# Performance work log

Measured on AMD Instinct MI355X. Metric: run time of the kernel, lower is better.

Reference implementation:

```python
import jax, jax.numpy as jnp
import numpy as np
from jax import lax

IMG_SIZE = 1024
NUM_CLASSES = 80
TOP_K = 300          # self.top_k
CLS_THRES = 0.05     # self.cls_thres
IOU_THR = 0.5        # nms overlap
BBOX_STD = jnp.array([0.1, 0.1, 0.2, 0.2], dtype=jnp.float32)


def make_anchors(img_size=IMG_SIZE):
    """Standard RetinaNet anchors: P3-P7, 3 ratios x 3 scales per cell."""
    strides = [8, 16, 32, 64, 128]
    ratios = np.array([0.5, 1.0, 2.0])
    scales = 2.0 ** (np.arange(3) / 3.0)
    out = []
    for s in strides:
        base = 4.0 * s
        ws, hs = [], []
        for r in ratios:
            for sc in scales:
                ws.append(base * sc / np.sqrt(r))
                hs.append(base * sc * np.sqrt(r))
        ws = np.array(ws); hs = np.array(hs)  # [9]
        fs = img_size // s
        shift = (np.arange(fs) + 0.5) * s
        cy, cx = np.meshgrid(shift, shift, indexing='ij')
        cx = cx.ravel()[:, None]; cy = cy.ravel()[:, None]
        a = np.stack([cx - ws / 2, cy - hs / 2, cx + ws / 2, cy + hs / 2], axis=-1)
        out.append(a.reshape(-1, 4))
    return np.concatenate(out, axis=0).astype(np.float32)  # [A,4]


def setup_inputs() -> dict:
    key = jax.random.key(0)
    k1, k2 = jax.random.split(key)
    anchors = jnp.asarray(make_anchors())[None]          # [1,A,4]
    A = anchors.shape[1]
    classifications = jax.random.uniform(k1, (1, A, NUM_CLASSES), dtype=jnp.float32)
    regressions = jax.random.normal(k2, (1, A, 4), dtype=jnp.float32)
    return {"classifications": classifications, "regressions": regressions,
            "anchors": anchors, "img_h": IMG_SIZE, "img_w": IMG_SIZE}


def decode_boxes(anchors, regressions):
    # BBoxTransform: mean=0, std=[.1,.1,.2,.2]
    w = anchors[..., 2] - anchors[..., 0]
    h = anchors[..., 3] - anchors[..., 1]
    cx = anchors[..., 0] + 0.5 * w
    cy = anchors[..., 1] + 0.5 * h
    d = regressions * BBOX_STD
    pcx = cx + d[..., 0] * w
    pcy = cy + d[..., 1] * h
    pw = jnp.exp(d[..., 2]) * w
    ph = jnp.exp(d[..., 3]) * h
    return jnp.stack([pcx - 0.5 * pw, pcy - 0.5 * ph,
                      pcx + 0.5 * pw, pcy + 0.5 * ph], axis=-1)


def pairwise_iou(b):  # b: [K,4]
    x1, y1, x2, y2 = b[:, 0], b[:, 1], b[:, 2], b[:, 3]
    area = jnp.clip(x2 - x1, 0) * jnp.clip(y2 - y1, 0)
    iw = jnp.clip(jnp.minimum(x2[:, None], x2[None]) - jnp.maximum(x1[:, None], x1[None]), 0)
    ih = jnp.clip(jnp.minimum(y2[:, None], y2[None]) - jnp.maximum(y1[:, None], y1[None]), 0)
    inter = iw * ih
    return inter / (area[:, None] + area[None] - inter + 1e-8)


def nms_one_class(boxes, scores_c):
    """Greedy NMS over top-K candidates above threshold for one class."""
    s = jnp.where(scores_c > CLS_THRES, scores_c, -jnp.inf)
    top_scores, top_idx = lax.top_k(s, TOP_K)        # sorted descending
    cand_valid = top_scores > CLS_THRES
    iou = pairwise_iou(boxes[top_idx])               # [K,K]
    idxs = jnp.arange(TOP_K)

    def body(suppressed, i):
        sup_i = suppressed[i] | (~cand_valid[i])
        new_sup = suppressed | ((~sup_i) & (iou[i] > IOU_THR) & (idxs > i))
        return new_sup, ~sup_i

    _, keep = lax.scan(body, jnp.zeros(TOP_K, bool), idxs)
    return top_idx, top_scores, keep


def reference(classifications, regressions, anchors, img_h, img_w):
    boxes = decode_boxes(anchors, regressions)       # [1,A,4]
    boxes = jnp.stack([jnp.maximum(boxes[..., 0], 0.0),
                       jnp.maximum(boxes[..., 1], 0.0),
                       jnp.minimum(boxes[..., 2], float(img_w)),
                       jnp.minimum(boxes[..., 3], float(img_h))], axis=-1)
    boxes0 = boxes[0]                                # [A,4]  (batch item 0, as original)
    cls0 = classifications[0]                        # [A,C]
    A, C = cls0.shape

    # per-class NMS, vmapped over the class axis
    top_idx, top_scores, keep = jax.vmap(nms_one_class, in_axes=(None, 1))(boxes0, cls0)
    # scatter kept scores back into dense [A,C] matrix (original 'scores' tensor)
    scores_mat = jnp.zeros((A, C), cls0.dtype).at[top_idx, jnp.arange(C)[:, None]].set(
        jnp.where(keep, top_scores, 0.0))

    scores_max = scores_mat.max(axis=1)
    labels = scores_mat.argmax(axis=1)
    valid = scores_max > 0
    # fixed-shape (jit-friendly) equivalent of the original's boolean filtering:
    final_scores = jnp.where(valid, scores_max, 0.0)
    final_labels = jnp.where(valid, labels, -1)
    final_boxes = jnp.where(valid[:, None], boxes0, 0.0)
    return final_scores, final_labels, final_boxes
```

## Files before the change

kernel.cpp:

```cpp
#include <hip/hip_runtime.h>
#include <cstdint>

typedef unsigned long long u64;
typedef unsigned int u32;

#define CLS_T    0.05f
#define T1G      0.9965f
#define TOPK     300
#define NWORDS   5
#define HBINS    2560
#define KEY_BASE 0x3D000000u
#define CCAP     1024
#define NBLK     2048
#define SCAP     16
#define OVBIT    0x80000000u

__device__ inline u32 bin_of_bits(u32 bits) {
    u32 b = (bits - KEY_BASE) >> 14;
    if (b > (HBINS - 1)) b = HBINS - 1;
    return b;
}

__device__ inline void cex(u64& v, u64 p, bool lo, bool up) {
    u64 mx = v > p ? v : p;
    u64 mn = v > p ? p : v;
    v = (lo == up) ? mx : mn;
}
__device__ inline void sstep(u64& a0, u64& a1, u32 tid, u32 kk, u32 j) {
    u64 p0 = __shfl_xor((unsigned long long)a0, (int)j, 64);
    u64 p1 = __shfl_xor((unsigned long long)a1, (int)j, 64);
    bool lo = ((tid & j) == 0);
    cex(a0, p0, lo, ((tid & kk) == 0));
    cex(a1, p1, lo, (((tid + 512u) & kk) == 0));
}
__device__ inline void lstep640(u64* cand, u64& a0, u64& a1, u32 tid, u32 kk, u32 j) {
    __syncthreads();
    if (tid < 512) { cand[tid] = a0; cand[tid + 512] = a1; }
    __syncthreads();
    if (tid < 512) {
        u64 p0 = cand[tid ^ j], p1 = cand[(tid ^ j) + 512];
        bool lo = ((tid & j) == 0);
        cex(a0, p0, lo, ((tid & kk) == 0));
        cex(a1, p1, lo, (((tid + 512u) & kk) == 0));
    }
}

__global__ void decode_kernel(const float* __restrict__ anc,
                              const float* __restrict__ reg,
                              const int* __restrict__ ph,
                              const int* __restrict__ pw,
                              float* __restrict__ boxes,
                              u64* __restrict__ akey, int A)
{
    int a = blockIdx.x * blockDim.x + threadIdx.x;
    if (a >= A) return;
    akey[a] = 0;
    float x1 = anc[a*4+0], y1 = anc[a*4+1], x2 = anc[a*4+2], y2 = anc[a*4+3];
    float w = x2 - x1, h = y2 - y1;
    float cx = x1 + 0.5f*w, cy = y1 + 0.5f*h;
    float r0 = reg[a*4+0]*0.1f, r1 = reg[a*4+1]*0.1f;
    float r2 = reg[a*4+2]*0.2f, r3 = reg[a*4+3]*0.2f;
    float pcx = cx + r0*w, pcy = cy + r1*h;
    float pw_ = expf(r2)*w, ph_ = expf(r3)*h;
    float W = (float)(*pw), H = (float)(*ph);
    boxes[a*4+0] = fmaxf(pcx - 0.5f*pw_, 0.0f);
    boxes[a*4+1] = fmaxf(pcy - 0.5f*ph_, 0.0f);
    boxes[a*4+2] = fminf(pcx + 0.5f*pw_, W);
    boxes[a*4+3] = fminf(pcy + 0.5f*ph_, H);
}

__global__ __launch_bounds__(256) void fused_scan_kernel(
    const float* __restrict__ anc, const float* __restrict__ reg,
    const int* __restrict__ ph, const int* __restrict__ pw,
    const float* __restrict__ cls,
    float* __restrict__ boxes, u64* __restrict__ akey,
    u64* __restrict__ gbuf, u32* __restrict__ segcnt, int A)
{
    const int tid = threadIdx.x;
    const int blk = blockIdx.x;

    float W = (float)(*pw), H = (float)(*ph);
    for (int a = blk * 256 + tid; a < A; a += NBLK * 256) {
        akey[a] = 0;
        float x1 = anc[a*4+0], y1 = anc[a*4+1], x2 = anc[a*4+2], y2 = anc[a*4+3];
        float w = x2 - x1, h = y2 - y1;
        float cx = x1 + 0.5f*w, cy = y1 + 0.5f*h;
        float r0 = reg[a*4+0]*0.1f, r1 = reg[a*4+1]*0.1f;
        float r2 = reg[a*4+2]*0.2f, r3 = reg[a*4+3]*0.2f;
        float pcx = cx + r0*w, pcy = cy + r1*h;
        float pw_ = expf(r2)*w, ph_ = expf(r3)*h;
        boxes[a*4+0] = fmaxf(pcx - 0.5f*pw_, 0.0f);
        boxes[a*4+1] = fmaxf(pcy - 0.5f*ph_, 0.0f);
        boxes[a*4+2] = fminf(pcx + 0.5f*pw_, W);
        boxes[a*4+3] = fminf(pcy + 0.5f*ph_, H);
    }

    __shared__ u32 cnt[80];
    __shared__ u64 buf[80][SCAP];
    __shared__ u32 s_over;
    for (int i = tid; i < 80; i += 256) cnt[i] = 0;
    if (tid == 0) s_over = 0;
    __syncthreads();

    size_t Nf4 = (size_t)A * 20;
    const float4* p4 = (const float4*)cls;
    for (size_t i = (size_t)blk * 256 + tid; i < Nf4; i += (size_t)NBLK * 256) {
        float4 v = p4[i];
        float ss[4] = {v.x, v.y, v.z, v.w};
        #pragma unroll
        for (int q = 0; q < 4; ++q) {
            if (ss[q] > T1G) {
                u32 flat = (u32)(i * 4 + q);
                u32 a = flat / 80u;
                u32 c = flat - a * 80u;
                u32 p = atomicAdd(&cnt[c], 1u);
                if (p < SCAP) buf[c][p] = ((u64)__float_as_uint(ss[q]) << 32) | (u32)(~a);
                else s_over = 1;
            }
        }
    }
    __syncthreads();

    const u32 ob = s_over ? OVBIT : 0u;
    for (int m = tid; m < 80 * SCAP; m += 256) {
        int c = m / SCAP, e = m - c * SCAP;
        u32 cc = cnt[c]; if (cc > SCAP) cc = SCAP;
        if ((u32)e < cc)
            gbuf[((size_t)c * NBLK + blk) * SCAP + e] = buf[c][e];
    }
    for (int c = tid; c < 80; c += 256) {
        u32 cc = cnt[c]; if (cc > SCAP) cc = SCAP;
        segcnt[(size_t)c * NBLK + blk] = cc | ob;
    }
}

__global__ __launch_bounds__(256) void prefix_kernel(
    const u32* __restrict__ segcnt, u32* __restrict__ pref,
    u32* __restrict__ totals)
{
    const int c = blockIdx.x;
    const int tid = threadIdx.x;
    __shared__ u32 part[256];
    __shared__ u32 s_ob;
    if (tid == 0) s_ob = 0;
    __syncthreads();

    const u32* row = segcnt + (size_t)c * NBLK;
    u32 v[8];
    u32 s = 0, ob = 0;
    #pragma unroll
    for (int q = 0; q < 8; ++q) {
        u32 r = row[tid * 8 + q];
        ob |= r & OVBIT;
        v[q] = r & ~OVBIT;
        s += v[q];
    }
    if (ob) atomicOr(&s_ob, 1u);
    part[tid] = s;
    __syncthreads();
    for (int d = 1; d < 256; d <<= 1) {
        u32 t = (tid >= d) ? part[tid - d] : 0;
        __syncthreads();
        part[tid] += t;
        __syncthreads();
    }
    u32 running = part[tid] - s;
    u32* prow = pref + (size_t)c * NBLK;
    #pragma unroll
    for (int q = 0; q < 8; ++q) { prow[tid * 8 + q] = running; running += v[q]; }
    if (tid == 255) totals[c] = part[255] | (s_ob ? OVBIT : 0u);
}

__global__ __launch_bounds__(640) void class_fused_kernel(
    const u32* __restrict__ totals, const u32* __restrict__ pref,
    const u64* __restrict__ gbuf,
    const float* __restrict__ cls,
    const float* __restrict__ boxes, u64* __restrict__ akey, int A, int C)
{
    const int c = blockIdx.x;
    const u32 tid = threadIdx.x;
    const int lane = tid & 63;

    __shared__ u32 sh[HBINS];
    __shared__ u32 sp[NBLK];
    __shared__ u64 cand[CCAP];
    __shared__ u32 s_sel, s_cnt, s_rem;
    __shared__ float4 sbox[TOPK];
    __shared__ float  sbar[TOPK];
    __shared__ u64 iomaskT[NWORDS][TOPK];
    __shared__ u64 s_keep[NWORDS];

    if (tid == 0) { s_sel = 0; s_cnt = 0; }
    __syncthreads();

    const u32 traw = totals[c];
    const bool over = (traw & OVBIT) != 0;
    const u32 n = traw & ~OVBIT;
    u32 cnt_f = 0;
    bool fast_ok = false;

    if (!over && n >= TOPK && n <= CCAP) {
        for (int i = tid; i < NBLK; i += 640) sp[i] = pref[(size_t)c * NBLK + i];
        __syncthreads();
        for (u32 i = tid; i < n; i += 640) {
            int lo = 0, hi = NBLK;
            while (hi - lo > 1) {
                int mid = (lo + hi) >> 1;
                if (sp[mid] <= i) lo = mid; else hi = mid;
            }
            u32 e = i - sp[lo];
            cand[i] = gbuf[((size_t)c * NBLK + lo) * SCAP + e];
        }
        __syncthreads();
        cnt_f = n;
        fast_ok = true;
    }

    if (!fast_ok) {
        __syncthreads();
        for (int i = tid; i < HBINS; i += 640) sh[i] = 0;
        if (tid == 0) s_cnt = 0;
        __syncthreads();
        for (int a = tid; a < A; a += 640) {
            float s = cls[(size_t)a * C + c];
            if (s > CLS_T) atomicAdd(&sh[bin_of_bits(__float_as_uint(s))], 1u);
        }
        __syncthreads();
        if (tid == 0) {
            u32 cum = 0; int sel = 0;
            for (int d = HBINS - 1; d >= 0; --d) {
                u32 nc = cum + sh[d];
                if (nc >= TOPK) { sel = d; break; }
                cum = nc;
            }
            s_sel = (u32)sel; s_rem = TOPK - cum;
        }
        __syncthreads();
        const u32 sel1 = s_sel;
        __syncthreads();
        for (int i = tid; i < 256; i += 640) sh[i] = 0;
        __syncthreads();
        for (int a = tid; a < A; a += 640) {
            float s = cls[(size_t)a * C + c];
            if (s > CLS_T) {
                u32 k = __float_as_uint(s) - KEY_BASE;
                u32 b = k >> 14; if (b >= HBINS) b = HBINS - 1;
                if (b == sel1) atomicAdd(&sh[(k >> 6) & 0xFF], 1u);
            }
        }
        __syncthreads();
        if (tid == 0) {
            u32 rem = s_rem, cum = 0; int sel = 0;
            for (int d = 255; d >= 0; --d) {
                u32 nc = cum + sh[d];
                if (nc >= rem) { sel = d; break; }
                cum = nc;
            }
            s_sel = (sel1 << 14) | ((u32)sel << 6);
            s_cnt = 0;
        }
        __syncthreads();
        const u32 thresh = s_sel;
        for (int a = tid; a < A; a += 640) {
            float s = cls[(size_t)a * C + c];
            if (s > CLS_T) {
                u32 bits = __float_as_uint(s);
                if (bits - KEY_BASE >= thresh) {
                    u32 p = atomicAdd(&s_cnt, 1u);
                    if (p < CCAP) cand[p] = ((u64)bits << 32) | (u32)(~(u32)a);
                }
            }
        }
        __syncthreads();
        cnt_f = s_cnt < CCAP ? s_cnt : CCAP;
    }

    for (u32 i = cnt_f + tid; i < CCAP; i += 640) cand[i] = 0;
    for (int m = tid; m < NWORDS * TOPK; m += 640) ((u64*)iomaskT)[m] = 0;
    __syncthreads();

    u64 a0 = 0, a1 = 0;
    if (tid < 512) { a0 = cand[tid]; a1 = cand[tid + 512]; }
    if (tid < 512)
        for (u32 kk = 2; kk <= 64; kk <<= 1)
            for (u32 j = kk >> 1; j >= 1; j >>= 1)
                sstep(a0, a1, tid, kk, j);
    lstep640(cand, a0, a1, tid, 128u, 64u);
    if (tid < 512) for (u32 j = 32; j >= 1; j >>= 1) sstep(a0, a1, tid, 128u, j);
    lstep640(cand, a0, a1, tid, 256u, 128u);
    lstep640(cand, a0, a1, tid, 256u, 64u);
    if (tid < 512) for (u32 j = 32; j >= 1; j >>= 1) sstep(a0, a1, tid, 256u, j);
    lstep640(cand, a0, a1, tid, 512u, 256u);
    lstep640(cand, a0, a1, tid, 512u, 128u);
    lstep640(cand, a0, a1, tid, 512u, 64u);
    if (tid < 512) for (u32 j = 32; j >= 1; j >>= 1) sstep(a0, a1, tid, 512u, j);
    if (tid < 512) {
        u64 mx = a0 > a1 ? a0 : a1, mn = a0 > a1 ? a1 : a0;
        a0 = mx; a1 = mn;
    }
    lstep640(cand, a0, a1, tid, 1024u, 256u);
    lstep640(cand, a0, a1, tid, 1024u, 128u);
    lstep640(cand, a0, a1, tid, 1024u, 64u);
    if (tid < 512) for (u32 j = 32; j >= 1; j >>= 1) sstep(a0, a1, tid, 1024u, j);

    const int T = (int)(cnt_f < TOPK ? cnt_f : TOPK);

    u64 key = a0; u32 aidx = 0;
    if ((int)tid < T) {
        aidx = ~(u32)(key & 0xFFFFFFFFull);
        float4 b4 = *(const float4*)(boxes + (size_t)aidx * 4);
        sbox[tid] = b4;
        sbar[tid] = fmaxf(b4.z - b4.x, 0.0f) * fmaxf(b4.w - b4.y, 0.0f);
    }
    __syncthreads();

    {
        const int jj = (int)(tid < 320 ? tid : tid - 320);
        const int p  = (int)(tid < 320 ? 0 : 1);
        if (jj < T) {
            float4 b = sbox[jj];
            float ar = sbar[jj];
            u64 cm[NWORDS] = {0,0,0,0,0};
            for (int i = p; i < jj; i += 2) {
                float4 bi = sbox[i];
                float iw = fmaxf(fminf(b.z, bi.z) - fmaxf(b.x, bi.x), 0.0f);
                float ih = fmaxf(fminf(b.w, bi.w) - fmaxf(b.y, bi.y), 0.0f);
                float inter = iw * ih;
                float uni = ((ar + sbar[i]) - inter) + 1e-8f;
                if (inter / uni > 0.5f) cm[i >> 6] |= 1ull << (i & 63);
            }
            #pragma unroll
            for (int w = 0; w < NWORDS; ++w)
                if (cm[w]) atomicOr(&iomaskT[w][jj], cm[w]);
        }
    }
    __syncthreads();

    if (tid < 64) {
        u64 K[NWORDS];
        #pragma unroll
        for (int w = 0; w < NWORDS; ++w) {
            int b = w * 64 + lane;
            bool valid = (b < T);
            u64 cmw = 0, se = 0;
            if (valid) {
                #pragma unroll
                for (int w2 = 0; w2 < NWORDS; ++w2)
                    if (w2 < w) se |= K[w2] & iomaskT[w2][b];
                cmw = iomaskT[w][b];
            }
            u64 U = __ballot(valid && se == 0);
            u64 Kw = 0;
            int guard = 0;
            while (U && guard++ < 64) {
                u64 newk = __ballot(((U >> lane) & 1ull) && ((cmw & U) == 0));
                Kw |= newk; U &= ~newk;
                u64 supp = __ballot((cmw & Kw) != 0);
                U &= ~supp;
            }
            K[w] = Kw;
        }
        if (lane == 0) {
            #pragma unroll
            for (int w = 0; w < NWORDS; ++w) s_keep[w] = K[w];
        }
    }
    __syncthreads();

    if ((int)tid < T) {
        if ((s_keep[tid >> 6] >> (tid & 63)) & 1ull) {
            u32 sbits = (u32)(key >> 32);
            u64 outk = ((u64)sbits << 32) | (u32)(255 - c);
            atomicMax(&akey[aidx], outk);
        }
    }
}

__global__ void finalize_kernel(const u64* __restrict__ akey,
                                float* __restrict__ out, int A)
{
    int a = blockIdx.x * blockDim.x + threadIdx.x;
    if (a >= A) return;
    float* scores = out;
    float* labels = out + A;
    float* boxes  = out + (size_t)2 * A;
    u64 k = akey[a];
    if (k) {
        scores[a] = __uint_as_float((u32)(k >> 32));
        labels[a] = (float)(int)(255u - (u32)(k & 0xFFFFFFFFull));
    } else {
        scores[a] = 0.0f;
        labels[a] = -1.0f;
        boxes[(size_t)a*4+0] = 0.0f;
        boxes[(size_t)a*4+1] = 0.0f;
        boxes[(size_t)a*4+2] = 0.0f;
        boxes[(size_t)a*4+3] = 0.0f;
    }
}

#define FB_CAP 1024
__global__ __launch_bounds__(256) void fb_topk_nms_kernel(
    const float* __restrict__ cls,
    const float* __restrict__ boxes,
    u64* __restrict__ akey,
    int A, int C)
{
    const int c   = blockIdx.x;
    const int tid = threadIdx.x;

    __shared__ u32 hist[HBINS];
    __shared__ u64 cand[FB_CAP];
    __shared__ float bx1[TOPK], by1[TOPK], bx2[TOPK], by2[TOPK], bar[TOPK];
    __shared__ u64 iomask[TOPK][NWORDS];
    __shared__ u64 keepm[NWORDS];
    __shared__ u32 s_sel1, s_sel2, s_rem, s_cnt;

    for (int i = tid; i < HBINS; i += 256) hist[i] = 0;
    __syncthreads();
    for (int a = tid; a < A; a += 256) {
        float s = cls[(size_t)a * C + c];
        if (s > CLS_T) {
            u32 k = __float_as_uint(s) - KEY_BASE;
            u32 b = k >> 14; if (b >= HBINS) b = HBINS - 1;
            atomicAdd(&hist[b], 1u);
        }
    }
    __syncthreads();
    if (tid == 0) {
        u32 cum = 0; int sel = 0;
        for (int d = HBINS - 1; d >= 0; --d) {
            u32 nc = cum + hist[d];
            if (nc >= TOPK) { sel = d; break; }
            cum = nc;
        }
        s_sel1 = (u32)sel; s_rem = TOPK - cum;
    }
    __syncthreads();
    const u32 sel1 = s_sel1;

    for (int i = tid; i < 256; i += 256) hist[i] = 0;
    __syncthreads();
    for (int a = tid; a < A; a += 256) {
        float s = cls[(size_t)a * C + c];
        if (s > CLS_T) {
            u32 k = __float_as_uint(s) - KEY_BASE;
            u32 b = k >> 14; if (b >= HBINS) b = HBINS - 1;
            if (b == sel1) atomicAdd(&hist[(k >> 6) & 0xFF], 1u);
        }
    }
    __syncthreads();
    if (tid == 0) {
        u32 rem = s_rem, cum = 0; int sel = 0;
        for (int d = 255; d >= 0; --d) {
            u32 nc = cum + hist[d];
            if (nc >= rem) { sel = d; break; }
            cum = nc;
        }
        s_sel2 = (u32)sel; s_cnt = 0;
    }
    __syncthreads();
    const u32 thresh = (sel1 << 14) | (s_sel2 << 6);

    for (int a = tid; a < A; a += 256) {
        float s = cls[(size_t)a * C + c];
        if (s > CLS_T) {
            u32 bits = __float_as_uint(s);
            u32 k = bits - KEY_BASE;
            if (k >= thresh) {
                u32 pos = atomicAdd(&s_cnt, 1u);
                if (pos < FB_CAP) cand[pos] = ((u64)bits << 32) | (u32)(~(u32)a);
            }
        }
    }
    __syncthreads();
    const u32 total = s_cnt < FB_CAP ? s_cnt : FB_CAP;
    for (int i = tid; i < FB_CAP; i += 256)
        if (i >= (int)total) cand[i] = 0;
    __syncthreads();

    for (u32 kk = 2; kk <= FB_CAP; kk <<= 1) {
        for (u32 j = kk >> 1; j > 0; j >>= 1) {
            for (u32 i = tid; i < FB_CAP; i += 256) {
                u32 l = i ^ j;
                if (l > i) {
                    u64 av = cand[i], bv = cand[l];
                    bool up = ((i & kk) == 0);
                    if ((up && av < bv) || (!up && av > bv)) { cand[i] = bv; cand[l] = av; }
                }
            }
            __syncthreads();
        }
    }
    const int T = (int)(total < TOPK ? total : TOPK);

    for (int i = tid; i < T; i += 256) {
        u32 a = ~(u32)(cand[i] & 0xFFFFFFFFull);
        float x1 = boxes[(size_t)a*4+0], y1 = boxes[(size_t)a*4+1];
        float x2 = boxes[(size_t)a*4+2], y2 = boxes[(size_t)a*4+3];
        bx1[i] = x1; by1[i] = y1; bx2[i] = x2; by2[i] = y2;
        bar[i] = fmaxf(x2 - x1, 0.0f) * fmaxf(y2 - y1, 0.0f);
    }
    __syncthreads();

    for (int i = tid; i < T; i += 256) {
        u64 m[NWORDS] = {0,0,0,0,0};
        float x1 = bx1[i], y1 = by1[i], x2 = bx2[i], y2 = by2[i], ai = bar[i];
        for (int j = i + 1; j < T; ++j) {
            float iw = fmaxf(fminf(x2, bx2[j]) - fmaxf(x1, bx1[j]), 0.0f);
            float ih = fmaxf(fminf(y2, by2[j]) - fmaxf(y1, by1[j]), 0.0f);
            float inter = iw * ih;
            float uni = ((ai + bar[j]) - inter) + 1e-8f;
            if (inter / uni > 0.5f) m[j >> 6] |= 1ull << (j & 63);
        }
        for (int k2 = 0; k2 < NWORDS; ++k2) iomask[i][k2] = m[k2];
    }
    __syncthreads();

    if (tid == 0) {
        u64 sup[NWORDS] = {0,0,0,0,0};
        u64 kp [NWORDS] = {0,0,0,0,0};
        for (int i = 0; i < T; ++i) {
            if (!((sup[i >> 6] >> (i & 63)) & 1ull)) {
                kp[i >> 6] |= 1ull << (i & 63);
                for (int k2 = 0; k2 < NWORDS; ++k2) sup[k2] |= iomask[i][k2];
            }
        }
        for (int k2 = 0; k2 < NWORDS; ++k2) keepm[k2] = kp[k2];
    }
    __syncthreads();

    for (int i = tid; i < T; i += 256) {
        if ((keepm[i >> 6] >> (i & 63)) & 1ull) {
            u64 key = cand[i];
            u32 a = ~(u32)(key & 0xFFFFFFFFull);
            u32 sbits = (u32)(key >> 32);
            u64 outk = ((u64)sbits << 32) | (u32)(255 - c);
            atomicMax(&akey[a], outk);
        }
    }
}

extern "C" void kernel_launch(void* const* d_in, const int* in_sizes, int n_in,
                              void* d_out, int out_size, void* d_ws, size_t ws_size,
                              hipStream_t stream) {
    const float* cls = (const float*)d_in[0];
    const float* reg = (const float*)d_in[1];
    const float* anc = (const float*)d_in[2];
    const int*   ph  = (const int*)d_in[3];
    const int*   pw  = (const int*)d_in[4];

    int A = in_sizes[2] / 4;
    int C = in_sizes[0] / A;

    float* out       = (float*)d_out;
    float* out_boxes = out + (size_t)2 * A;

    size_t akey_bytes = (size_t)A * sizeof(u64);
    size_t off_sc     = (akey_bytes + 255) & ~(size_t)255;
    size_t sc_bytes   = (size_t)80 * NBLK * sizeof(u32);
    size_t off_pf     = (off_sc + sc_bytes + 255) & ~(size_t)255;
    size_t off_tt     = (off_pf + sc_bytes + 255) & ~(size_t)255;
    size_t tt_bytes   = 80 * sizeof(u32);
    size_t off_gb     = (off_tt + tt_bytes + 255) & ~(size_t)255;
    size_t gb_bytes   = (size_t)80 * NBLK * SCAP * sizeof(u64);
    size_t need       = off_gb + gb_bytes;

    u64* akey = (u64*)d_ws;

    bool fastpath = (C == 80) && ((A & 3) == 0) && (A < (1 << 20)) && (ws_size >= need);

    if (fastpath) {
        u32* segcnt = (u32*)((char*)d_ws + off_sc);
        u32* pref   = (u32*)((char*)d_ws + off_pf);
        u32* totals = (u32*)((char*)d_ws + off_tt);
        u64* gbuf   = (u64*)((char*)d_ws + off_gb);

        fused_scan_kernel<<<NBLK, 256, 0, stream>>>(anc, reg, ph, pw, cls,
                                                    out_boxes, akey, gbuf, segcnt, A);
        prefix_kernel<<<80, 256, 0, stream>>>(segcnt, pref, totals);
        class_fused_kernel<<<C, 640, 0, stream>>>(totals, pref, gbuf, cls, out_boxes, akey, A, C);
    } else {
        decode_kernel<<<(A + 255) / 256, 256, 0, stream>>>(anc, reg, ph, pw, out_boxes, akey, A);
        fb_topk_nms_kernel<<<C, 256, 0, stream>>>(cls, out_boxes, akey, A, C);
    }

    finalize_kernel<<<(A + 255) / 256, 256, 0, stream>>>(akey, out, A);
}
```

Before: 59.52 us.

## Fold prefix scan into class kernel and decode boxes lazily

Removes the separate prefix_kernel launch by computing the per-class segment prefix sum inside class_fused_kernel with a 512-thread shared-memory scan. Box decoding moves out of the scan kernel and happens on demand: class_fused_kernel decodes only its candidate boxes, and finalize decodes boxes only for anchors that kept a score. This cuts one launch and the full boxes write and reread, at the cost of repeated decode work per class and a longer serial prologue in the class kernel.

```diff
diff --git a/kernel.cpp b/kernel.cpp
--- a/kernel.cpp
+++ b/kernel.cpp
@@ -21,6 +21,26 @@
     return b;
 }
 
+__device__ inline float4 decode_box(const float* __restrict__ anc,
+                                    const float* __restrict__ reg,
+                                    u32 a, float W, float H)
+{
+    float x1 = anc[(size_t)a*4+0], y1 = anc[(size_t)a*4+1];
+    float x2 = anc[(size_t)a*4+2], y2 = anc[(size_t)a*4+3];
+    float w = x2 - x1, h = y2 - y1;
+    float cx = x1 + 0.5f*w, cy = y1 + 0.5f*h;
+    float r0 = reg[(size_t)a*4+0]*0.1f, r1 = reg[(size_t)a*4+1]*0.1f;
+    float r2 = reg[(size_t)a*4+2]*0.2f, r3 = reg[(size_t)a*4+3]*0.2f;
+    float pcx = cx + r0*w, pcy = cy + r1*h;
+    float pw_ = expf(r2)*w, ph_ = expf(r3)*h;
+    float4 b;
+    b.x = fmaxf(pcx - 0.5f*pw_, 0.0f);
+    b.y = fmaxf(pcy - 0.5f*ph_, 0.0f);
+    b.z = fminf(pcx + 0.5f*pw_, W);
+    b.w = fminf(pcy + 0.5f*ph_, H);
+    return b;
+}
+
 __device__ inline void cex(u64& v, u64 p, bool lo, bool up) {
     u64 mx = v > p ? v : p;
     u64 mn = v > p ? p : v;
@@ -55,45 +75,21 @@
     int a = blockIdx.x * blockDim.x + threadIdx.x;
     if (a >= A) return;
     akey[a] = 0;
-    float x1 = anc[a*4+0], y1 = anc[a*4+1], x2 = anc[a*4+2], y2 = anc[a*4+3];
-    float w = x2 - x1, h = y2 - y1;
-    float cx = x1 + 0.5f*w, cy = y1 + 0.5f*h;
-    float r0 = reg[a*4+0]*0.1f, r1 = reg[a*4+1]*0.1f;
-    float r2 = reg[a*4+2]*0.2f, r3 = reg[a*4+3]*0.2f;
-    float pcx = cx + r0*w, pcy = cy + r1*h;
-    float pw_ = expf(r2)*w, ph_ = expf(r3)*h;
     float W = (float)(*pw), H = (float)(*ph);
-    boxes[a*4+0] = fmaxf(pcx - 0.5f*pw_, 0.0f);
-    boxes[a*4+1] = fmaxf(pcy - 0.5f*ph_, 0.0f);
-    boxes[a*4+2] = fminf(pcx + 0.5f*pw_, W);
-    boxes[a*4+3] = fminf(pcy + 0.5f*ph_, H);
+    float4 b = decode_box(anc, reg, (u32)a, W, H);
+    boxes[a*4+0] = b.x; boxes[a*4+1] = b.y;
+    boxes[a*4+2] = b.z; boxes[a*4+3] = b.w;
 }
 
 __global__ __launch_bounds__(256) void fused_scan_kernel(
-    const float* __restrict__ anc, const float* __restrict__ reg,
-    const int* __restrict__ ph, const int* __restrict__ pw,
     const float* __restrict__ cls,
-    float* __restrict__ boxes, u64* __restrict__ akey,
+    u64* __restrict__ akey,
     u64* __restrict__ gbuf, u32* __restrict__ segcnt, int A)
 {
     const int tid = threadIdx.x;
     const int blk = blockIdx.x;
 
-    float W = (float)(*pw), H = (float)(*ph);
-    for (int a = blk * 256 + tid; a < A; a += NBLK * 256) {
-        akey[a] = 0;
-        float x1 = anc[a*4+0], y1 = anc[a*4+1], x2 = anc[a*4+2], y2 = anc[a*4+3];
-        float w = x2 - x1, h = y2 - y1;
-        float cx = x1 + 0.5f*w, cy = y1 + 0.5f*h;
-        float r0 = reg[a*4+0]*0.1f, r1 = reg[a*4+1]*0.1f;
-        float r2 = reg[a*4+2]*0.2f, r3 = reg[a*4+3]*0.2f;
-        float pcx = cx + r0*w, pcy = cy + r1*h;
-        float pw_ = expf(r2)*w, ph_ = expf(r3)*h;
-        boxes[a*4+0] = fmaxf(pcx - 0.5f*pw_, 0.0f);
-        boxes[a*4+1] = fmaxf(pcy - 0.5f*ph_, 0.0f);
-        boxes[a*4+2] = fminf(pcx + 0.5f*pw_, W);
-        boxes[a*4+3] = fminf(pcy + 0.5f*ph_, H);
-    }
+    for (int a = blk * 256 + tid; a < A; a += NBLK * 256) akey[a] = 0;
 
     __shared__ u32 cnt[80];
     __shared__ u64 buf[80][SCAP];
@@ -134,48 +130,12 @@
     }
 }
 
-__global__ __launch_bounds__(256) void prefix_kernel(
-    const u32* __restrict__ segcnt, u32* __restrict__ pref,
-    u32* __restrict__ totals)
-{
-    const int c = blockIdx.x;
-    const int tid = threadIdx.x;
-    __shared__ u32 part[256];
-    __shared__ u32 s_ob;
-    if (tid == 0) s_ob = 0;
-    __syncthreads();
-
-    const u32* row = segcnt + (size_t)c * NBLK;
-    u32 v[8];
-    u32 s = 0, ob = 0;
-    #pragma unroll
-    for (int q = 0; q < 8; ++q) {
-        u32 r = row[tid * 8 + q];
-        ob |= r & OVBIT;
-        v[q] = r & ~OVBIT;
-        s += v[q];
-    }
-    if (ob) atomicOr(&s_ob, 1u);
-    part[tid] = s;
-    __syncthreads();
-    for (int d = 1; d < 256; d <<= 1) {
-        u32 t = (tid >= d) ? part[tid - d] : 0;
-        __syncthreads();
-        part[tid] += t;
-        __syncthreads();
-    }
-    u32 running = part[tid] - s;
-    u32* prow = pref + (size_t)c * NBLK;
-    #pragma unroll
-    for (int q = 0; q < 8; ++q) { prow[tid * 8 + q] = running; running += v[q]; }
-    if (tid == 255) totals[c] = part[255] | (s_ob ? OVBIT : 0u);
-}
-
 __global__ __launch_bounds__(640) void class_fused_kernel(
-    const u32* __restrict__ totals, const u32* __restrict__ pref,
-    const u64* __restrict__ gbuf,
+    const u32* __restrict__ segcnt, const u64* __restrict__ gbuf,
     const float* __restrict__ cls,
-    const float* __restrict__ boxes, u64* __restrict__ akey, int A, int C)
+    const float* __restrict__ anc, const float* __restrict__ reg,
+    const int* __restrict__ ph, const int* __restrict__ pw,
+    u64* __restrict__ akey, int A, int C)
 {
     const int c = blockIdx.x;
     const u32 tid = threadIdx.x;
@@ -184,24 +144,53 @@
     __shared__ u32 sh[HBINS];
     __shared__ u32 sp[NBLK];
     __shared__ u64 cand[CCAP];
-    __shared__ u32 s_sel, s_cnt, s_rem;
+    __shared__ u32 s_sel, s_cnt, s_rem, s_ob;
     __shared__ float4 sbox[TOPK];
     __shared__ float  sbar[TOPK];
     __shared__ u64 iomaskT[NWORDS][TOPK];
     __shared__ u64 s_keep[NWORDS];
 
-    if (tid == 0) { s_sel = 0; s_cnt = 0; }
-    __syncthreads();
-
-    const u32 traw = totals[c];
-    const bool over = (traw & OVBIT) != 0;
-    const u32 n = traw & ~OVBIT;
+    if (tid == 0) { s_sel = 0; s_cnt = 0; s_ob = 0; }
+    __syncthreads();
+
+    const float W = (float)(*pw), H = (float)(*ph);
+
+    u32 v[4] = {0,0,0,0};
+    u32 s = 0;
+    if (tid < 512) {
+        const u32* row = segcnt + (size_t)c * NBLK;
+        u32 ob = 0;
+        #pragma unroll
+        for (int q = 0; q < 4; ++q) {
+            u32 r = row[tid * 4 + q];
+            ob |= r & OVBIT;
+            v[q] = r & ~OVBIT;
+            s += v[q];
+        }
+        if (ob) atomicOr(&s_ob, 1u);
+        sh[tid] = s;
+    }
+    __syncthreads();
+    for (int d = 1; d < 512; d <<= 1) {
+        u32 t2 = (tid >= (u32)d && tid < 512) ? sh[tid - d] : 0;
+        __syncthreads();
+        if (tid < 512) sh[tid] += t2;
+        __syncthreads();
+    }
+    if (tid < 512) {
+        u32 run = sh[tid] - s;
+        #pragma unroll
+        for (int q = 0; q < 4; ++q) { sp[tid * 4 + q] = run; run += v[q]; }
+    }
+    __syncthreads();
+    const u32 n = sh[511];
+    const bool over = (s_ob != 0);
+    __syncthreads();
+
     u32 cnt_f = 0;
     bool fast_ok = false;
 
     if (!over && n >= TOPK && n <= CCAP) {
-        for (int i = tid; i < NBLK; i += 640) sp[i] = pref[(size_t)c * NBLK + i];
-        __syncthreads();
         for (u32 i = tid; i < n; i += 640) {
             int lo = 0, hi = NBLK;
             while (hi - lo > 1) {
@@ -222,8 +211,8 @@
         if (tid == 0) s_cnt = 0;
         __syncthreads();
         for (int a = tid; a < A; a += 640) {
-            float s = cls[(size_t)a * C + c];
-            if (s > CLS_T) atomicAdd(&sh[bin_of_bits(__float_as_uint(s))], 1u);
+            float sc = cls[(size_t)a * C + c];
+            if (sc > CLS_T) atomicAdd(&sh[bin_of_bits(__float_as_uint(sc))], 1u);
         }
         __syncthreads();
         if (tid == 0) {
@@ -241,9 +230,9 @@
         for (int i = tid; i < 256; i += 640) sh[i] = 0;
         __syncthreads();
         for (int a = tid; a < A; a += 640) {
-            float s = cls[(size_t)a * C + c];
-            if (s > CLS_T) {
-                u32 k = __float_as_uint(s) - KEY_BASE;
+            float sc = cls[(size_t)a * C + c];
+            if (sc > CLS_T) {
+                u32 k = __float_as_uint(sc) - KEY_BASE;
                 u32 b = k >> 14; if (b >= HBINS) b = HBINS - 1;
                 if (b == sel1) atomicAdd(&sh[(k >> 6) & 0xFF], 1u);
             }
@@ -262,9 +251,9 @@
         __syncthreads();
         const u32 thresh = s_sel;
         for (int a = tid; a < A; a += 640) {
-            float s = cls[(size_t)a * C + c];
-            if (s > CLS_T) {
-                u32 bits = __float_as_uint(s);
+            float sc = cls[(size_t)a * C + c];
+            if (sc > CLS_T) {
+                u32 bits = __float_as_uint(sc);
                 if (bits - KEY_BASE >= thresh) {
                     u32 p = atomicAdd(&s_cnt, 1u);
                     if (p < CCAP) cand[p] = ((u64)bits << 32) | (u32)(~(u32)a);
@@ -308,7 +297,7 @@
     u64 key = a0; u32 aidx = 0;
     if ((int)tid < T) {
         aidx = ~(u32)(key & 0xFFFFFFFFull);
-        float4 b4 = *(const float4*)(boxes + (size_t)aidx * 4);
+        float4 b4 = decode_box(anc, reg, aidx, W, H);
         sbox[tid] = b4;
         sbar[tid] = fmaxf(b4.z - b4.x, 0.0f) * fmaxf(b4.w - b4.y, 0.0f);
     }
@@ -377,7 +366,37 @@
 }
 
 __global__ void finalize_kernel(const u64* __restrict__ akey,
+                                const float* __restrict__ anc,
+                                const float* __restrict__ reg,
+                                const int* __restrict__ ph,
+                                const int* __restrict__ pw,
                                 float* __restrict__ out, int A)
+{
+    int a = blockIdx.x * blockDim.x + threadIdx.x;
+    if (a >= A) return;
+    float* scores = out;
+    float* labels = out + A;
+    float* boxes  = out + (size_t)2 * A;
+    u64 k = akey[a];
+    if (k) {
+        scores[a] = __uint_as_float((u32)(k >> 32));
+        labels[a] = (float)(int)(255u - (u32)(k & 0xFFFFFFFFull));
+        float W = (float)(*pw), H = (float)(*ph);
+        float4 b = decode_box(anc, reg, (u32)a, W, H);
+        boxes[(size_t)a*4+0] = b.x; boxes[(size_t)a*4+1] = b.y;
+        boxes[(size_t)a*4+2] = b.z; boxes[(size_t)a*4+3] = b.w;
+    } else {
+        scores[a] = 0.0f;
+        labels[a] = -1.0f;
+        boxes[(size_t)a*4+0] = 0.0f;
+        boxes[(size_t)a*4+1] = 0.0f;
+        boxes[(size_t)a*4+2] = 0.0f;
+        boxes[(size_t)a*4+3] = 0.0f;
+    }
+}
+
+__global__ void fb_finalize_kernel(const u64* __restrict__ akey,
+                                   float* __restrict__ out, int A)
 {
     int a = blockIdx.x * blockDim.x + threadIdx.x;
     if (a >= A) return;
@@ -558,10 +577,7 @@
     size_t akey_bytes = (size_t)A * sizeof(u64);
     size_t off_sc     = (akey_bytes + 255) & ~(size_t)255;
     size_t sc_bytes   = (size_t)80 * NBLK * sizeof(u32);
-    size_t off_pf     = (off_sc + sc_bytes + 255) & ~(size_t)255;
-    size_t off_tt     = (off_pf + sc_bytes + 255) & ~(size_t)255;
-    size_t tt_bytes   = 80 * sizeof(u32);
-    size_t off_gb     = (off_tt + tt_bytes + 255) & ~(size_t)255;
+    size_t off_gb     = (off_sc + sc_bytes + 255) & ~(size_t)255;
     size_t gb_bytes   = (size_t)80 * NBLK * SCAP * sizeof(u64);
     size_t need       = off_gb + gb_bytes;
 
@@ -571,18 +587,14 @@
 
     if (fastpath) {
         u32* segcnt = (u32*)((char*)d_ws + off_sc);
-        u32* pref   = (u32*)((char*)d_ws + off_pf);
-        u32* totals = (u32*)((char*)d_ws + off_tt);
         u64* gbuf   = (u64*)((char*)d_ws + off_gb);
 
-        fused_scan_kernel<<<NBLK, 256, 0, stream>>>(anc, reg, ph, pw, cls,
-                                                    out_boxes, akey, gbuf, segcnt, A);
-        prefix_kernel<<<80, 256, 0, stream>>>(segcnt, pref, totals);
-        class_fused_kernel<<<C, 640, 0, stream>>>(totals, pref, gbuf, cls, out_boxes, akey, A, C);
+        fused_scan_kernel<<<NBLK, 256, 0, stream>>>(cls, akey, gbuf, segcnt, A);
+        class_fused_kernel<<<C, 640, 0, stream>>>(segcnt, gbuf, cls, anc, reg, ph, pw, akey, A, C);
+        finalize_kernel<<<(A + 255) / 256, 256, 0, stream>>>(akey, anc, reg, ph, pw, out, A);
     } else {
         decode_kernel<<<(A + 255) / 256, 256, 0, stream>>>(anc, reg, ph, pw, out_boxes, akey, A);
         fb_topk_nms_kernel<<<C, 256, 0, stream>>>(cls, out_boxes, akey, A, C);
-    }
-
-    finalize_kernel<<<(A + 255) / 256, 256, 0, stream>>>(akey, out, A);
-}
+        fb_finalize_kernel<<<(A + 255) / 256, 256, 0, stream>>>(akey, out, A);
+    }
+}
```

Result: faster. 57.27 us (-3.8%).
